# Kernel tuning notes

Hardware: AMD Instinct MI355X
Metric: run time of the kernel (lower is better)

## Reference

```python
import jax, jax.numpy as jnp
import numpy as np
from jax import lax

S, V, E, H, T = 2048, 50257, 512, 1024, 12
HD = H // 2  # per-direction hidden
START, END = 0, 1
NEG = -1e6


def setup_inputs() -> dict:
    key = jax.random.key(0)
    ks = jax.random.split(key, 16)
    sentence = jax.random.randint(ks[0], (S,), 0, V)
    gold_tags = jax.random.randint(ks[1], (S,), 2, T)  # avoid START/END gold labels
    emb = jax.random.normal(ks[2], (V, E), jnp.float32) * 0.1
    s = 0.05
    wih_f = jax.random.normal(ks[3], (4 * HD, E), jnp.float32) * s
    whh_f = jax.random.normal(ks[4], (4 * HD, HD), jnp.float32) * s
    b_f = jax.random.normal(ks[5], (4 * HD,), jnp.float32) * s
    wih_b = jax.random.normal(ks[6], (4 * HD, E), jnp.float32) * s
    whh_b = jax.random.normal(ks[7], (4 * HD, HD), jnp.float32) * s
    b_b = jax.random.normal(ks[8], (4 * HD,), jnp.float32) * s
    w_out = jax.random.normal(ks[9], (T, H), jnp.float32) * s
    b_out = jax.random.normal(ks[10], (T,), jnp.float32) * s
    transitions = jax.random.normal(ks[11], (T, T), jnp.float32)
    transitions = transitions.at[START, :].set(NEG).at[:, END].set(NEG)
    h0 = jax.random.normal(ks[12], (2, HD), jnp.float32)
    c0 = jax.random.normal(ks[13], (2, HD), jnp.float32)
    return dict(sentence=sentence, gold_tags=gold_tags, emb=emb,
                wih_f=wih_f, whh_f=whh_f, b_f=b_f,
                wih_b=wih_b, whh_b=whh_b, b_b=b_b,
                w_out=w_out, b_out=b_out, transitions=transitions,
                h0=h0, c0=c0)


def _lstm_dir(x, h0, c0, wih, whh, b):
    # x: [S, E] -> hidden states [S, HD]; PyTorch gate order i,f,g,o
    def step(carry, xt):
        h, c = carry
        g = xt @ wih.T + h @ whh.T + b
        i, f, gg, o = jnp.split(g, 4)
        i, f, o = jax.nn.sigmoid(i), jax.nn.sigmoid(f), jax.nn.sigmoid(o)
        c = f * c + i * jnp.tanh(gg)
        h = o * jnp.tanh(c)
        return (h, c), h
    _, hs = lax.scan(step, (h0, c0), x)
    return hs


def _feats(sentence, emb, wih_f, whh_f, b_f, wih_b, whh_b, b_b, w_out, b_out, h0, c0):
    x = emb[sentence]                                  # [S, E]
    hf = _lstm_dir(x, h0[0], c0[0], wih_f, whh_f, b_f)  # [S, HD]
    hb = _lstm_dir(x[::-1], h0[1], c0[1], wih_b, whh_b, b_b)[::-1]
    return jnp.concatenate([hf, hb], axis=1) @ w_out.T + b_out  # [S, T]


def _crf_nll(feats, gold_tags, transitions):
    # forward algorithm (log partition)
    init = jnp.full((T,), NEG, feats.dtype).at[START].set(0.0)
    def step(prev, feat):
        nxt = jax.nn.logsumexp(prev[None, :] + transitions + feat[:, None], axis=1)
        return nxt, None
    final, _ = lax.scan(step, init, feats)
    alpha = jax.nn.logsumexp(final + transitions[END])
    # gold score
    tags = jnp.concatenate([jnp.array([START], gold_tags.dtype), gold_tags])
    trans_score = jnp.sum(transitions[tags[1:], tags[:-1]])
    emit_score = jnp.sum(feats[jnp.arange(feats.shape[0]), tags[1:]])
    gold = trans_score + emit_score + transitions[END, tags[-1]]
    return alpha - gold


def reference(sentence, gold_tags, emb, wih_f, whh_f, b_f, wih_b, whh_b, b_b,
              w_out, b_out, transitions, h0, c0):
    feats = _feats(sentence, emb, wih_f, whh_f, b_f, wih_b, whh_b, b_b,
                   w_out, b_out, h0, c0)
    return _crf_nll(feats, gold_tags, transitions)
```

## Files before the change

kernel.cpp:

```cpp
#include <hip/hip_runtime.h>
#include <hip/hip_bf16.h>

#define S 2048
#define HD 512
#define EDIM 512
#define NT 12
#define G4 2048
#define NWGD 64
#define RPW 32
#define JPW 8
#define HSTR 36

typedef unsigned short ushort_t;
typedef unsigned int uint_t;

__device__ __forceinline__ ushort_t f2b(float f) {
    uint_t u = __float_as_uint(f);
    uint_t r = u + 0x7fffu + ((u >> 16) & 1u);
    return (ushort_t)(r >> 16);
}
__device__ __forceinline__ float b2f(ushort_t h) {
    return __uint_as_float(((uint_t)h) << 16);
}
__device__ __forceinline__ float sigm(float x) { return 1.f / (1.f + __expf(-x)); }
__device__ __forceinline__ float tanh_(float x) {
    float e = __expf(2.f * x);
    return 1.f - 2.f / (e + 1.f);
}

__global__ __launch_bounds__(256, 2)
void xw_gemm(const int* __restrict__ sentence, const float* __restrict__ emb,
             const float* __restrict__ wih_f, const float* __restrict__ b_f,
             const float* __restrict__ wih_b, const float* __restrict__ b_b,
             ushort_t* __restrict__ xw) {
    __shared__ float As[32][68];
    __shared__ float Bs[32][68];
    __shared__ int toks[64];
    const int tid = threadIdx.x;
    const int tbase = blockIdx.x * 64;
    const int rbase = blockIdx.y * 64;
    const int dir = blockIdx.z;
    const float* wih = dir ? wih_b : wih_f;
    const float* bia = dir ? b_b : b_f;
    if (tid < 64) {
        int tt = tbase + tid;
        toks[tid] = sentence[dir ? (S - 1 - tt) : tt];
    }
    __syncthreads();
    const int lm = tid >> 2;
    const int lk = (tid & 3) * 8;
    const int ty = tid >> 4, tx = tid & 15;
    const float* aBase = emb + (size_t)toks[lm] * EDIM + lk;
    const float* bBase = wih + (size_t)(rbase + lm) * EDIM + lk;
    float acc[4][4];
#pragma unroll
    for (int i = 0; i < 4; ++i)
#pragma unroll
        for (int j = 0; j < 4; ++j) acc[i][j] = 0.f;

    for (int kc = 0; kc < EDIM; kc += 32) {
        float4 a0 = ((const float4*)(aBase + kc))[0];
        float4 a1 = ((const float4*)(aBase + kc))[1];
        float4 b0 = ((const float4*)(bBase + kc))[0];
        float4 b1 = ((const float4*)(bBase + kc))[1];
        __syncthreads();
        As[lk + 0][lm] = a0.x; As[lk + 1][lm] = a0.y; As[lk + 2][lm] = a0.z; As[lk + 3][lm] = a0.w;
        As[lk + 4][lm] = a1.x; As[lk + 5][lm] = a1.y; As[lk + 6][lm] = a1.z; As[lk + 7][lm] = a1.w;
        Bs[lk + 0][lm] = b0.x; Bs[lk + 1][lm] = b0.y; Bs[lk + 2][lm] = b0.z; Bs[lk + 3][lm] = b0.w;
        Bs[lk + 4][lm] = b1.x; Bs[lk + 5][lm] = b1.y; Bs[lk + 6][lm] = b1.z; Bs[lk + 7][lm] = b1.w;
        __syncthreads();
#pragma unroll
        for (int kk = 0; kk < 32; ++kk) {
            float4 a4 = *(const float4*)&As[kk][ty * 4];
            float4 b4 = *(const float4*)&Bs[kk][tx * 4];
            float av[4] = {a4.x, a4.y, a4.z, a4.w};
            float bv[4] = {b4.x, b4.y, b4.z, b4.w};
#pragma unroll
            for (int i = 0; i < 4; ++i)
#pragma unroll
                for (int j = 0; j < 4; ++j) acc[i][j] = fmaf(av[i], bv[j], acc[i][j]);
        }
    }
    float4 bi = *(const float4*)&bia[rbase + tx * 4];
    float bvv[4] = {bi.x, bi.y, bi.z, bi.w};
#pragma unroll
    for (int i = 0; i < 4; ++i) {
        ushort4 o;
        o.x = f2b(acc[i][0] + bvv[0]);
        o.y = f2b(acc[i][1] + bvv[1]);
        o.z = f2b(acc[i][2] + bvv[2]);
        o.w = f2b(acc[i][3] + bvv[3]);
        ushort_t* p = xw + ((size_t)dir * S + tbase + ty * 4 + i) * G4 + rbase + tx * 4;
        *(ushort4*)p = o;
    }
}

__global__ __launch_bounds__(256, 1)
void lstm_rec(const float* __restrict__ whh_f, const float* __restrict__ whh_b,
              const float* __restrict__ h0, const float* __restrict__ c0,
              const ushort_t* __restrict__ xw, float* hs) {
    __shared__ float hstage[16 * HSTR];
    __shared__ float gates[RPW];
    const int tid = threadIdx.x;
    const int dir = blockIdx.x >> 6;
    const int wg = blockIdx.x & 63;
    const int jbase = wg * JPW;
    const int rg = tid >> 4, kc = tid & 15;
    const float* whh = dir ? whh_b : whh_f;

    int grow[2];
#pragma unroll
    for (int ri = 0; ri < 2; ++ri) {
        int r = rg * 2 + ri;
        grow[ri] = (r >> 3) * HD + jbase + (r & 7);
    }
    float4 w[2][8];
#pragma unroll
    for (int ri = 0; ri < 2; ++ri)
#pragma unroll
        for (int i = 0; i < 8; ++i)
            w[ri][i] = *(const float4*)&whh[(size_t)grow[ri] * HD + kc * 32 + i * 4];

    const ushort_t* xwd = xw + (size_t)dir * S * G4;
    float* hsd = hs + (size_t)dir * S * HD;

    float cj = 0.f;
    if (tid < JPW) cj = c0[dir * HD + jbase + tid];

    {
        int c = tid >> 4, m = (2 * tid) & 31;
        hstage[c * HSTR + m] = h0[dir * HD + 2 * tid];
        hstage[c * HSTR + m + 1] = h0[dir * HD + 2 * tid + 1];
    }
    __syncthreads();

    const bool isw = (kc == 0);
    for (int t = 0; t < S; ++t) {
        float xv0 = 0.f, xv1 = 0.f;
        if (isw) {
            xv0 = b2f(xwd[(size_t)t * G4 + grow[0]]);
            xv1 = b2f(xwd[(size_t)t * G4 + grow[1]]);
        }
        float a0 = 0.f, a1 = 0.f;
#pragma unroll
        for (int i = 0; i < 8; ++i) {
            float4 h4 = *(const float4*)&hstage[kc * HSTR + i * 4];
            a0 = fmaf(w[0][i].x, h4.x, a0); a0 = fmaf(w[0][i].y, h4.y, a0);
            a0 = fmaf(w[0][i].z, h4.z, a0); a0 = fmaf(w[0][i].w, h4.w, a0);
            a1 = fmaf(w[1][i].x, h4.x, a1); a1 = fmaf(w[1][i].y, h4.y, a1);
            a1 = fmaf(w[1][i].z, h4.z, a1); a1 = fmaf(w[1][i].w, h4.w, a1);
        }
#pragma unroll
        for (int m = 1; m < 16; m <<= 1) {
            a0 += __shfl_xor(a0, m);
            a1 += __shfl_xor(a1, m);
        }
        if (isw) {
            gates[rg * 2] = a0 + xv0;
            gates[rg * 2 + 1] = a1 + xv1;
        }
        __syncthreads();
        if (tid < JPW) {
            float ai = gates[tid], af = gates[JPW + tid];
            float ag = gates[2 * JPW + tid], ao = gates[3 * JPW + tid];
            float ii = sigm(ai), ff = sigm(af), gg = tanh_(ag), oo = sigm(ao);
            cj = ff * cj + ii * gg;
            float hnew = oo * tanh_(cj);
            __hip_atomic_store(&hsd[(size_t)t * HD + jbase + tid], hnew,
                               __ATOMIC_RELAXED, __HIP_MEMORY_SCOPE_AGENT);
        }
        if (t < S - 1) {
            const unsigned long long* p0 =
                (const unsigned long long*)&hsd[(size_t)t * HD + 2 * tid];
            float v0, v1;
            for (;;) {
                unsigned long long v =
                    __hip_atomic_load(p0, __ATOMIC_RELAXED, __HIP_MEMORY_SCOPE_AGENT);
                uint_t lo = (uint_t)v, hi = (uint_t)(v >> 32);
                if (lo != 0xFFFFFFFFu && hi != 0xFFFFFFFFu) {
                    v0 = __uint_as_float(lo);
                    v1 = __uint_as_float(hi);
                    break;
                }
            }
            int c = tid >> 4, m = (2 * tid) & 31;
            hstage[c * HSTR + m] = v0;
            hstage[c * HSTR + m + 1] = v1;
        }
        __syncthreads();
    }
}

__global__ __launch_bounds__(256)
void feats_k(const float* __restrict__ hs, const float* __restrict__ w_out,
             const float* __restrict__ b_out, float* __restrict__ feats) {
    const int t = blockIdx.x, tid = threadIdx.x;
    float4 h4;
    if (tid < 128)
        h4 = *(const float4*)&hs[(size_t)t * HD + tid * 4];
    else
        h4 = *(const float4*)&hs[(size_t)S * HD + (size_t)(S - 1 - t) * HD + (tid - 128) * 4];
    float acc[NT];
#pragma unroll
    for (int tg = 0; tg < NT; ++tg) {
        float4 w4 = *(const float4*)&w_out[(size_t)tg * 1024 + tid * 4];
        acc[tg] = h4.x * w4.x + h4.y * w4.y + h4.z * w4.z + h4.w * w4.w;
    }
#pragma unroll
    for (int m = 1; m < 64; m <<= 1)
#pragma unroll
        for (int tg = 0; tg < NT; ++tg) acc[tg] += __shfl_xor(acc[tg], m);
    __shared__ float part[4][NT];
    if ((tid & 63) == 0) {
#pragma unroll
        for (int tg = 0; tg < NT; ++tg) part[tid >> 6][tg] = acc[tg];
    }
    __syncthreads();
    if (tid < NT)
        feats[(size_t)t * NT + tid] =
            part[0][tid] + part[1][tid] + part[2][tid] + part[3][tid] + b_out[tid];
}

__global__ __launch_bounds__(256, 1)
void crf_k(const float* __restrict__ feats, const int* __restrict__ gold,
           const float* __restrict__ trans, float* __restrict__ out) {
    extern __shared__ float sfeats[];
    __shared__ float red[256];
    __shared__ float nprev[NT];
    __shared__ float tr[144];
    __shared__ float gold_sh;
    const int tid = threadIdx.x;
    for (int i = tid; i < S * NT / 4; i += 256)
        ((float4*)sfeats)[i] = ((const float4*)feats)[i];
    if (tid < 144) tr[tid] = trans[tid];
    __syncthreads();
    float gsum = 0.f;
    for (int t = tid; t < S; t += 256) {
        int a = gold[t];
        int b = t ? gold[t - 1] : 0;
        gsum += tr[a * NT + b] + sfeats[t * NT + a];
    }
    red[tid] = gsum;
    __syncthreads();
    for (int s = 128; s; s >>= 1) {
        if (tid < s) red[tid] += red[tid + s];
        __syncthreads();
    }
    if (tid == 0) gold_sh = red[0] + tr[1 * NT + gold[S - 1]];
    __syncthreads();
    const int i = tid >> 4, j = tid & 15;
    const bool act = (tid < 192) && (j < NT);
    float tij = act ? tr[i * NT + j] : -3e38f;
    float prev = (j == 0) ? 0.f : -1e6f;
    for (int t = 0; t < S; ++t) {
        float v = act ? (prev + tij) : -3e38f;
        float mx = v;
        mx = fmaxf(mx, __shfl_xor(mx, 1));
        mx = fmaxf(mx, __shfl_xor(mx, 2));
        mx = fmaxf(mx, __shfl_xor(mx, 4));
        mx = fmaxf(mx, __shfl_xor(mx, 8));
        float e = __expf(v - mx);
        float ss = e;
        ss += __shfl_xor(ss, 1);
        ss += __shfl_xor(ss, 2);
        ss += __shfl_xor(ss, 4);
        ss += __shfl_xor(ss, 8);
        if (tid < 192 && j == 0) nprev[i] = mx + __logf(ss) + sfeats[t * NT + i];
        __syncthreads();
        prev = nprev[j < NT ? j : 0];
        __syncthreads();
    }
    if (tid < 64) {
        float v2 = (tid < NT) ? prev + tr[1 * NT + tid] : -3e38f;
        float mx = v2;
        mx = fmaxf(mx, __shfl_xor(mx, 1));
        mx = fmaxf(mx, __shfl_xor(mx, 2));
        mx = fmaxf(mx, __shfl_xor(mx, 4));
        mx = fmaxf(mx, __shfl_xor(mx, 8));
        float e = __expf(v2 - mx);
        float ss = e;
        ss += __shfl_xor(ss, 1);
        ss += __shfl_xor(ss, 2);
        ss += __shfl_xor(ss, 4);
        ss += __shfl_xor(ss, 8);
        if (tid == 0) out[0] = (mx + __logf(ss)) - gold_sh;
    }
}

extern "C" void kernel_launch(void* const* d_in, const int* in_sizes, int n_in,
                              void* d_out, int out_size, void* d_ws, size_t ws_size,
                              hipStream_t stream) {
    const int* sentence = (const int*)d_in[0];
    const int* gold = (const int*)d_in[1];
    const float* emb = (const float*)d_in[2];
    const float* wih_f = (const float*)d_in[3];
    const float* whh_f = (const float*)d_in[4];
    const float* b_f = (const float*)d_in[5];
    const float* wih_b = (const float*)d_in[6];
    const float* whh_b = (const float*)d_in[7];
    const float* b_b = (const float*)d_in[8];
    const float* w_out = (const float*)d_in[9];
    const float* b_out = (const float*)d_in[10];
    const float* trans = (const float*)d_in[11];
    const float* h0 = (const float*)d_in[12];
    const float* c0 = (const float*)d_in[13];
    float* out = (float*)d_out;

    char* ws = (char*)d_ws;
    const size_t XW_B = (size_t)2 * S * G4 * 2;
    const size_t HS_B = (size_t)2 * S * HD * 4;
    ushort_t* xw = (ushort_t*)ws;
    float* hs = (float*)(ws + XW_B);
    float* feats = (float*)(ws + XW_B + HS_B);

    hipMemsetAsync(hs, 0xFF, HS_B, stream);

    dim3 gg(S / 64, G4 / 64, 2);
    xw_gemm<<<gg, 256, 0, stream>>>(sentence, emb, wih_f, b_f, wih_b, b_b, xw);

    lstm_rec<<<2 * NWGD, 256, 0, stream>>>(whh_f, whh_b, h0, c0, xw, hs);

    feats_k<<<S, 256, 0, stream>>>(hs, w_out, b_out, feats);

    const size_t CRF_LDS = (size_t)S * NT * 4;
    hipFuncSetAttribute((const void*)crf_k,
                        hipFuncAttributeMaxDynamicSharedMemorySize, (int)CRF_LDS);
    crf_k<<<1, 256, CRF_LDS, stream>>>(feats, gold, trans, out);
}
```

Before: 5.409 ms.

## Repartition LSTM recurrence into fewer, larger workgroups with four rows per thread

The persistent recurrent kernel goes from 64 workgroups per direction (8 hidden units each, 256 threads) to 16 workgroups per direction (32 hidden units each, 512 threads). Each thread now keeps four weight rows in registers and loads its four input-projection values with one vector load. The aim is to cut the number of workgroups that poll and synchronise through global memory on every timestep. In exchange, each workgroup does more work per step on the critical path, and each thread holds more weight registers.

```diff
diff --git a/kernel.cpp b/kernel.cpp
--- a/kernel.cpp
+++ b/kernel.cpp
@@ -1,14 +1,13 @@
 #include <hip/hip_runtime.h>
-#include <hip/hip_bf16.h>
 
 #define S 2048
 #define HD 512
 #define EDIM 512
 #define NT 12
 #define G4 2048
-#define NWGD 64
-#define RPW 32
-#define JPW 8
+#define NWGD 16
+#define JPW 32
+#define RPW 128
 #define HSTR 36
 
 typedef unsigned short ushort_t;
@@ -95,31 +94,31 @@
     }
 }
 
-__global__ __launch_bounds__(256, 1)
+__global__ __launch_bounds__(512, 1)
 void lstm_rec(const float* __restrict__ whh_f, const float* __restrict__ whh_b,
               const float* __restrict__ h0, const float* __restrict__ c0,
               const ushort_t* __restrict__ xw, float* hs) {
     __shared__ float hstage[16 * HSTR];
     __shared__ float gates[RPW];
     const int tid = threadIdx.x;
-    const int dir = blockIdx.x >> 6;
-    const int wg = blockIdx.x & 63;
+    const int dir = blockIdx.x >> 4;
+    const int wg = blockIdx.x & 15;
     const int jbase = wg * JPW;
     const int rg = tid >> 4, kc = tid & 15;
     const float* whh = dir ? whh_b : whh_f;
 
-    int grow[2];
-#pragma unroll
-    for (int ri = 0; ri < 2; ++ri) {
-        int r = rg * 2 + ri;
-        grow[ri] = (r >> 3) * HD + jbase + (r & 7);
-    }
-    float4 w[2][8];
-#pragma unroll
-    for (int ri = 0; ri < 2; ++ri)
-#pragma unroll
-        for (int i = 0; i < 8; ++i)
-            w[ri][i] = *(const float4*)&whh[(size_t)grow[ri] * HD + kc * 32 + i * 4];
+    const int r0 = rg * 4;
+    const int g = r0 >> 5;
+    const int u0 = r0 & 31;
+    const size_t xwrow = (size_t)g * HD + jbase + u0;
+
+    float4 w[4][8];
+#pragma unroll
+    for (int ri = 0; ri < 4; ++ri) {
+        const float* wrow = whh + (size_t)(g * HD + jbase + u0 + ri) * HD + kc * 32;
+#pragma unroll
+        for (int i = 0; i < 8; ++i) w[ri][i] = *(const float4*)(wrow + i * 4);
+    }
 
     const ushort_t* xwd = xw + (size_t)dir * S * G4;
     float* hsd = hs + (size_t)dir * S * HD;
@@ -127,7 +126,7 @@
     float cj = 0.f;
     if (tid < JPW) cj = c0[dir * HD + jbase + tid];
 
-    {
+    if (tid < 256) {
         int c = tid >> 4, m = (2 * tid) & 31;
         hstage[c * HSTR + m] = h0[dir * HD + 2 * tid];
         hstage[c * HSTR + m + 1] = h0[dir * HD + 2 * tid + 1];
@@ -136,12 +135,12 @@
 
     const bool isw = (kc == 0);
     for (int t = 0; t < S; ++t) {
-        float xv0 = 0.f, xv1 = 0.f;
+        float xv[4] = {0.f, 0.f, 0.f, 0.f};
         if (isw) {
-            xv0 = b2f(xwd[(size_t)t * G4 + grow[0]]);
-            xv1 = b2f(xwd[(size_t)t * G4 + grow[1]]);
-        }
-        float a0 = 0.f, a1 = 0.f;
+            ushort4 x4 = *(const ushort4*)&xwd[(size_t)t * G4 + xwrow];
+            xv[0] = b2f(x4.x); xv[1] = b2f(x4.y); xv[2] = b2f(x4.z); xv[3] = b2f(x4.w);
+        }
+        float a0 = 0.f, a1 = 0.f, a2 = 0.f, a3 = 0.f;
 #pragma unroll
         for (int i = 0; i < 8; ++i) {
             float4 h4 = *(const float4*)&hstage[kc * HSTR + i * 4];
@@ -149,15 +148,21 @@
             a0 = fmaf(w[0][i].z, h4.z, a0); a0 = fmaf(w[0][i].w, h4.w, a0);
             a1 = fmaf(w[1][i].x, h4.x, a1); a1 = fmaf(w[1][i].y, h4.y, a1);
             a1 = fmaf(w[1][i].z, h4.z, a1); a1 = fmaf(w[1][i].w, h4.w, a1);
+            a2 = fmaf(w[2][i].x, h4.x, a2); a2 = fmaf(w[2][i].y, h4.y, a2);
+            a2 = fmaf(w[2][i].z, h4.z, a2); a2 = fmaf(w[2][i].w, h4.w, a2);
+            a3 = fmaf(w[3][i].x, h4.x, a3); a3 = fmaf(w[3][i].y, h4.y, a3);
+            a3 = fmaf(w[3][i].z, h4.z, a3); a3 = fmaf(w[3][i].w, h4.w, a3);
         }
 #pragma unroll
         for (int m = 1; m < 16; m <<= 1) {
-            a0 += __shfl_xor(a0, m);
-            a1 += __shfl_xor(a1, m);
+            a0 += __shfl_xor(a0, m); a1 += __shfl_xor(a1, m);
+            a2 += __shfl_xor(a2, m); a3 += __shfl_xor(a3, m);
         }
         if (isw) {
-            gates[rg * 2] = a0 + xv0;
-            gates[rg * 2 + 1] = a1 + xv1;
+            gates[r0 + 0] = a0 + xv[0];
+            gates[r0 + 1] = a1 + xv[1];
+            gates[r0 + 2] = a2 + xv[2];
+            gates[r0 + 3] = a3 + xv[3];
         }
         __syncthreads();
         if (tid < JPW) {
@@ -169,7 +174,7 @@
             __hip_atomic_store(&hsd[(size_t)t * HD + jbase + tid], hnew,
                                __ATOMIC_RELAXED, __HIP_MEMORY_SCOPE_AGENT);
         }
-        if (t < S - 1) {
+        if (t < S - 1 && tid < 256) {
             const unsigned long long* p0 =
                 (const unsigned long long*)&hsd[(size_t)t * HD + 2 * tid];
             float v0, v1;
@@ -318,7 +323,7 @@
     dim3 gg(S / 64, G4 / 64, 2);
     xw_gemm<<<gg, 256, 0, stream>>>(sentence, emb, wih_f, b_f, wih_b, b_b, xw);
 
-    lstm_rec<<<2 * NWGD, 256, 0, stream>>>(whh_f, whh_b, h0, c0, xw, hs);
+    lstm_rec<<<2 * NWGD, 512, 0, stream>>>(whh_f, whh_b, h0, c0, xw, hs);
 
     feats_k<<<S, 256, 0, stream>>>(hs, w_out, b_out, feats);
 
```

New measurement: 5.247 ms. 3.0% less time.
